# Kernel tuning notes

Hardware: AMD Instinct MI355X
Metric: run time of the kernel (lower is better)

The kernel has to match this reference:

```python
import jax, jax.numpy as jnp
import numpy as np

D_MODEL = 1024
NUM_HEADS = 16
MAX_LEN = 512  # chunk_size
BATCH = 2
SEQ_LEN = 2048


def _mha(x, w_in, b_in, w_out, b_out, num_heads):
    """torch.nn.MultiheadAttention (eval mode, self-attn) over the last-but-one axis.
    x: (..., S, d). Packed in-proj weight w_in: (3d, d), out-proj w_out: (d, d)."""
    *batch, S, d = x.shape
    hd = d // num_heads
    qkv = x @ w_in.T + b_in                      # (..., S, 3d)
    q, k, v = jnp.split(qkv, 3, axis=-1)
    def heads(t):
        return t.reshape(*batch, S, num_heads, hd)
    q, k, v = heads(q), heads(k), heads(v)
    scale = 1.0 / np.sqrt(hd).astype(np.float32)
    scores = jnp.einsum('...qhd,...khd->...hqk', q, k) * scale
    attn = jax.nn.softmax(scores, axis=-1)
    o = jnp.einsum('...hqk,...khd->...qhd', attn, v).reshape(*batch, S, d)
    return o @ w_out.T + b_out


def setup_inputs() -> dict:
    key = jax.random.key(0)
    ks = jax.random.split(key, 5)
    d = D_MODEL
    s = 0.02
    return {
        'x': jax.random.normal(ks[0], (BATCH, SEQ_LEN, d), dtype=jnp.float32),
        'w_in_l': jax.random.normal(ks[1], (3 * d, d), dtype=jnp.float32) * s,
        'b_in_l': jnp.zeros((3 * d,), jnp.float32),
        'w_out_l': jax.random.normal(ks[2], (d, d), dtype=jnp.float32) * s,
        'b_out_l': jnp.zeros((d,), jnp.float32),
        'w_in_g': jax.random.normal(ks[3], (3 * d, d), dtype=jnp.float32) * s,
        'b_in_g': jnp.zeros((3 * d,), jnp.float32),
        'w_out_g': jax.random.normal(ks[4], (d, d), dtype=jnp.float32) * s,
        'b_out_g': jnp.zeros((d,), jnp.float32),
    }


def reference(x, w_in_l, b_in_l, w_out_l, b_out_l, w_in_g, b_in_g, w_out_g, b_out_g):
    B, S, d = x.shape
    cs = MAX_LEN
    nc = S // cs
    # (B, nc, cs, d) -> (B, cs, nc, d): for each intra-chunk position, attend across chunks.
    xc = x.reshape(B, nc, cs, d).transpose(0, 2, 1, 3)
    # Vectorized replacement for the python loop over chunk positions:
    # batched MHA with batch (B, cs) and sequence length nc.
    loc = _mha(xc, w_in_l, b_in_l, w_out_l, b_out_l, NUM_HEADS)  # (B, cs, nc, d)
    # Faithful to torch: stack -> (nc, cs, B, d), transpose(1,2) -> (nc, B, cs, d),
    # then raw reshape to (B, S, d) (a layout-reinterpreting view, preserved here).
    loc = loc.transpose(2, 0, 1, 3).reshape(B, S, d)
    # Global full self-attention over the whole sequence.
    return _mha(loc, w_in_g, b_in_g, w_out_g, b_out_g, NUM_HEADS)
```

## Files before the change

### kernel.cpp

```cpp
#include <hip/hip_runtime.h>

#define BB 2
#define SS 2048
#define DD 1024
#define HH 16
#define HD 64
#define CS 512
#define NC 4
#define TD 3072
#define MM 4096

typedef __attribute__((ext_vector_type(8))) short short8;
typedef __attribute__((ext_vector_type(4))) float floatx4;

__device__ __forceinline__ float bf2f(unsigned short h) {
  union { unsigned int u; float f; } v; v.u = ((unsigned int)h) << 16; return v.f;
}
__device__ __forceinline__ unsigned short f2bf(float f) {
  union { float f; unsigned int u; } v; v.f = f;
  unsigned int r = (v.u + 0x7fffu + ((v.u >> 16) & 1u)) >> 16;
  return (unsigned short)r;
}
__device__ __forceinline__ short8 ld8f(const float* p) {
  floatx4 f0 = *(const floatx4*)p;
  floatx4 f1 = *(const floatx4*)(p + 4);
  short8 o;
  o[0] = (short)f2bf(f0[0]); o[1] = (short)f2bf(f0[1]);
  o[2] = (short)f2bf(f0[2]); o[3] = (short)f2bf(f0[3]);
  o[4] = (short)f2bf(f1[0]); o[5] = (short)f2bf(f1[1]);
  o[6] = (short)f2bf(f1[2]); o[7] = (short)f2bf(f1[3]);
  return o;
}
__device__ __forceinline__ short8 scale8_eighth(short8 a) {
  short8 o;
#pragma unroll
  for (int j = 0; j < 8; ++j) o[j] = (short)f2bf(bf2f((unsigned short)a[j]) * 0.125f);
  return o;
}
__device__ __forceinline__ void async16(const void* g, void* l) {
  __builtin_amdgcn_global_load_lds((const __attribute__((address_space(1))) void*)g,
                                   (__attribute__((address_space(3))) void*)l, 16, 0, 0);
}

__global__ __launch_bounds__(256) void cvt_bf16(const float* __restrict__ in,
                                                unsigned short* __restrict__ out, int n) {
  int i = (blockIdx.x * 256 + threadIdx.x) * 8;
  if (i < n) *(short8*)(out + i) = ld8f(in + i);
}

template <int W_F32, int C_F32>
__global__ __launch_bounds__(256) void gemm_bt_bias(
    const unsigned short* __restrict__ A, const void* __restrict__ Wv,
    const float* __restrict__ bias, void* __restrict__ Cv, int M, int N, int K) {
  __shared__ unsigned short sA[128 * 32];
  __shared__ unsigned short sB[128 * 32];
  const int tid = threadIdx.x;
  const int wid = tid >> 6, lane = tid & 63;
  const int quad = lane >> 4, l15 = lane & 15;
  const int wm = wid & 1, wn = wid >> 1;
  const int bm = blockIdx.y, bn = blockIdx.x;

  floatx4 acc[4][4];
#pragma unroll
  for (int i = 0; i < 4; ++i)
#pragma unroll
    for (int j = 0; j < 4; ++j) acc[i][j] = (floatx4){0.f, 0.f, 0.f, 0.f};

  const int r = tid >> 2;
  const int kc = (tid & 3) * 8;
  const unsigned short* gA = A + (size_t)(bm * 128 + r) * K + kc;
  const float*          gWf = (const float*)Wv          + (size_t)(bn * 128 + r) * K + kc;
  const unsigned short* gWh = (const unsigned short*)Wv + (size_t)(bn * 128 + r) * K + kc;
  unsigned short* lA = sA + wid * 512;
  unsigned short* lB = sB + wid * 512;

  for (int k0 = 0; k0 < K; k0 += 32) {
    async16(gA + k0, lA);
    async16(gA + (size_t)64 * K + k0, lA + 2048);
    if (W_F32) {
      short8 b0 = ld8f(gWf + k0);
      short8 b1 = ld8f(gWf + (size_t)64 * K + k0);
      *(short8*)(sB + r * 32 + kc) = b0;
      *(short8*)(sB + (64 + r) * 32 + kc) = b1;
    } else {
      async16(gWh + k0, lB);
      async16(gWh + (size_t)64 * K + k0, lB + 2048);
    }
    __syncthreads();

    short8 af[4], bfr[4];
#pragma unroll
    for (int i = 0; i < 4; ++i)
      af[i] = *(const short8*)(sA + (wm * 64 + i * 16 + l15) * 32 + quad * 8);
#pragma unroll
    for (int j = 0; j < 4; ++j)
      bfr[j] = *(const short8*)(sB + (wn * 64 + j * 16 + l15) * 32 + quad * 8);
#pragma unroll
    for (int i = 0; i < 4; ++i)
#pragma unroll
      for (int j = 0; j < 4; ++j)
        acc[i][j] = __builtin_amdgcn_mfma_f32_16x16x32_bf16(af[i], bfr[j], acc[i][j], 0, 0, 0);
    __syncthreads();
  }

#pragma unroll
  for (int j = 0; j < 4; ++j) {
    int n = bn * 128 + wn * 64 + j * 16 + l15;
    float bv = bias[n];
#pragma unroll
    for (int i = 0; i < 4; ++i) {
      int mrow = bm * 128 + wm * 64 + i * 16 + quad * 4;
#pragma unroll
      for (int rr = 0; rr < 4; ++rr) {
        float v = acc[i][j][rr] + bv;
        if (C_F32) ((float*)Cv)[(size_t)(mrow + rr) * N + n] = v;
        else ((unsigned short*)Cv)[(size_t)(mrow + rr) * N + n] = f2bf(v);
      }
    }
  }
}

__global__ __launch_bounds__(256) void attn_local(const unsigned short* __restrict__ QKV,
                                                  unsigned short* __restrict__ O) {
  const int tid = threadIdx.x;
  const int wid = tid >> 6, lane = tid & 63;
  const int idx = blockIdx.x * 4 + wid;
  const int h = idx & 15, c = (idx >> 4) & 511, b = idx >> 13;

  float q[NC], k[NC], v[NC];
#pragma unroll
  for (int n = 0; n < NC; ++n) {
    size_t base = (size_t)(b * SS + n * CS + c) * TD + h * HD + lane;
    q[n] = bf2f(QKV[base]);
    k[n] = bf2f(QKV[base + DD]);
    v[n] = bf2f(QKV[base + 2 * DD]);
  }
  float s[NC][NC];
#pragma unroll
  for (int m = 0; m < NC; ++m)
#pragma unroll
    for (int n = 0; n < NC; ++n) {
      float p = q[m] * k[n];
#pragma unroll
      for (int off = 32; off >= 1; off >>= 1) p += __shfl_xor(p, off);
      s[m][n] = p * 0.125f;
    }
#pragma unroll
  for (int m = 0; m < NC; ++m) {
    float mx = fmaxf(fmaxf(s[m][0], s[m][1]), fmaxf(s[m][2], s[m][3]));
    float e[NC], sum = 0.f;
#pragma unroll
    for (int n = 0; n < NC; ++n) { e[n] = __expf(s[m][n] - mx); sum += e[n]; }
    float o = (e[0] * v[0] + e[1] * v[1] + e[2] * v[2] + e[3] * v[3]) / sum;
    O[(size_t)(m * (BB * CS) + b * CS + c) * DD + h * HD + lane] = f2bf(o);
  }
}

__global__ __launch_bounds__(256) void transpose_v(const unsigned short* __restrict__ QKV,
                                                   unsigned short* __restrict__ VT) {
  __shared__ unsigned short sT[64 * 64];
  const int tid = threadIdx.x;
  const int bh = blockIdx.x, b = bh >> 4, h = bh & 15;
  const int s0 = blockIdx.y * 64;
#pragma unroll
  for (int it = 0; it < 2; ++it) {
    int C = it * 256 + tid;
    int t = C >> 3, dc = C & 7;
    short8 v = *(const short8*)(QKV + (size_t)(b * SS + s0 + t) * TD + 2 * DD + h * HD + dc * 8);
    *(short8*)(sT + t * 64 + ((dc ^ (t & 7)) << 3)) = v;
  }
  __syncthreads();
#pragma unroll
  for (int it = 0; it < 2; ++it) {
    int C = it * 256 + tid;
    int d = C >> 3, tc = C & 7;
    short8 o;
#pragma unroll
    for (int j = 0; j < 8; ++j) {
      int t = tc * 8 + j;
      o[j] = (short)sT[t * 64 + (((d >> 3) ^ (t & 7)) << 3) + (d & 7)];
    }
    *(short8*)(VT + ((size_t)(bh * 64 + d)) * SS + s0 + tc * 8) = o;
  }
}

__global__ __launch_bounds__(128) void attn_global(
    const unsigned short* __restrict__ Q, const unsigned short* __restrict__ Kp,
    const unsigned short* __restrict__ VT, unsigned short* __restrict__ O) {
  __shared__ unsigned short sK[64 * 64];
  __shared__ unsigned short sVT[64 * 64];
  __shared__ unsigned short sP[2][32 * 64];
  const int tid = threadIdx.x;
  const int wid = tid >> 6, lane = tid & 63;
  const int quad = lane >> 4, l15 = lane & 15;
  const int bh = blockIdx.x;
  const int b = bh >> 4, h = bh & 15;
  const int q0 = blockIdx.y * 64 + wid * 32;

  short8 qf[2][2];
#pragma unroll
  for (int g = 0; g < 2; ++g) {
    const unsigned short* qr = Q + (size_t)(b * SS + q0 + g * 16 + l15) * TD + h * HD + quad * 8;
    qf[g][0] = scale8_eighth(*(const short8*)qr);
    qf[g][1] = scale8_eighth(*(const short8*)(qr + 32));
  }

  float lsum[2][4];
  floatx4 oacc[2][4];
#pragma unroll
  for (int g = 0; g < 2; ++g)
#pragma unroll
    for (int s = 0; s < 4; ++s) { lsum[g][s] = 0.f; oacc[g][s] = (floatx4){0.f, 0.f, 0.f, 0.f}; }

  unsigned short* myP = &sP[wid][0];
  const unsigned short* vbase = VT + (size_t)(bh * 64) * SS;

  for (int kt = 0; kt < SS / 64; ++kt) {
    const int kbase = kt * 64;
#pragma unroll
    for (int it = 0; it < 4; ++it) {
      int P = it * 128 + tid;
      int key = P >> 3, dc = P & 7;
      short8 kv = *(const short8*)(Kp + (size_t)(b * SS + kbase + key) * TD + h * HD + dc * 8);
      *(short8*)(sK + key * 64 + ((dc ^ (key & 7)) << 3)) = kv;
    }
#pragma unroll
    for (int it = 0; it < 4; ++it) {
      int P = it * 128 + tid;
      int dim = P >> 3, kcc = P & 7;
      short8 vv = *(const short8*)(vbase + (size_t)dim * SS + kbase + kcc * 8);
      *(short8*)(sVT + dim * 64 + ((kcc ^ (dim & 7)) << 3)) = vv;
    }
    __syncthreads();

    floatx4 sacc[2][4];
#pragma unroll
    for (int sub = 0; sub < 4; ++sub) {
      int key = sub * 16 + l15;
      int c0 = (quad ^ (key & 7)) << 3;
      short8 kf0 = *(const short8*)(sK + key * 64 + c0);
      short8 kf1 = *(const short8*)(sK + key * 64 + (c0 ^ 32));
#pragma unroll
      for (int g = 0; g < 2; ++g) {
        floatx4 z = (floatx4){0.f, 0.f, 0.f, 0.f};
        z = __builtin_amdgcn_mfma_f32_16x16x32_bf16(qf[g][0], kf0, z, 0, 0, 0);
        z = __builtin_amdgcn_mfma_f32_16x16x32_bf16(qf[g][1], kf1, z, 0, 0, 0);
        sacc[g][sub] = z;
      }
    }

#pragma unroll
    for (int g = 0; g < 2; ++g)
#pragma unroll
      for (int sub = 0; sub < 4; ++sub) {
        int kc8 = sub * 2 + (l15 >> 3), k7 = l15 & 7;
#pragma unroll
        for (int rr = 0; rr < 4; ++rr) {
          unsigned int u = __float_as_uint(__expf(sacc[g][sub][rr]));
          lsum[g][rr] += __uint_as_float(u & 0xffff0000u);
          int row = g * 16 + quad * 4 + rr;
          myP[row * 64 + ((kc8 ^ (row & 7)) << 3) + k7] = (unsigned short)(u >> 16);
        }
      }
    __asm__ volatile("s_waitcnt lgkmcnt(0)" ::: "memory");

    short8 pf[2][2];
#pragma unroll
    for (int g = 0; g < 2; ++g) {
      int row = g * 16 + l15;
      int sw = row & 7;
#pragma unroll
      for (int c = 0; c < 2; ++c)
        pf[g][c] = *(const short8*)(myP + row * 64 + (((c * 4 + quad) ^ sw) << 3));
    }

#pragma unroll
    for (int sub = 0; sub < 4; ++sub) {
      int n = sub * 16 + l15;
      int v0 = (quad ^ (n & 7)) << 3;
      short8 vt0 = *(const short8*)(sVT + n * 64 + v0);
      short8 vt1 = *(const short8*)(sVT + n * 64 + (v0 ^ 32));
#pragma unroll
      for (int g = 0; g < 2; ++g) {
        oacc[g][sub] = __builtin_amdgcn_mfma_f32_16x16x32_bf16(pf[g][0], vt0, oacc[g][sub], 0, 0, 0);
        oacc[g][sub] = __builtin_amdgcn_mfma_f32_16x16x32_bf16(pf[g][1], vt1, oacc[g][sub], 0, 0, 0);
      }
    }
    __syncthreads();
  }

  float linv[2][4];
#pragma unroll
  for (int g = 0; g < 2; ++g)
#pragma unroll
    for (int rr = 0; rr < 4; ++rr) {
      float t = lsum[g][rr];
#pragma unroll
      for (int off = 8; off >= 1; off >>= 1) t += __shfl_xor(t, off);
      linv[g][rr] = 1.f / t;
    }
#pragma unroll
  for (int g = 0; g < 2; ++g)
#pragma unroll
    for (int sub = 0; sub < 4; ++sub)
#pragma unroll
      for (int rr = 0; rr < 4; ++rr) {
        int row = b * SS + q0 + g * 16 + quad * 4 + rr;
        O[(size_t)row * DD + h * HD + sub * 16 + l15] = f2bf(oacc[g][sub][rr] * linv[g][rr]);
      }
}

extern "C" void kernel_launch(void* const* d_in, const int* in_sizes, int n_in,
                              void* d_out, int out_size, void* d_ws, size_t ws_size,
                              hipStream_t stream) {
  const float* x       = (const float*)d_in[0];
  const float* w_in_l  = (const float*)d_in[1];
  const float* b_in_l  = (const float*)d_in[2];
  const float* w_out_l = (const float*)d_in[3];
  const float* b_out_l = (const float*)d_in[4];
  const float* w_in_g  = (const float*)d_in[5];
  const float* b_in_g  = (const float*)d_in[6];
  const float* w_out_g = (const float*)d_in[7];
  const float* b_out_g = (const float*)d_in[8];

  unsigned short* wsA = (unsigned short*)d_ws;
  unsigned short* wsB = wsA + (size_t)MM * TD;
  unsigned short* dob = (unsigned short*)d_out;
  unsigned short* wbf_out_l = dob;
  unsigned short* wbf_in_g  = dob + (size_t)DD * DD;
  unsigned short* wbf_in_l  = dob + 4 * (size_t)DD * DD;
  unsigned short* o1        = dob + 4 * (size_t)DD * DD;
  unsigned short* vtbuf     = dob;

  dim3 blk(256);
  cvt_bf16<<<dim3(DD * DD / 2048), blk, 0, stream>>>(w_out_l, wbf_out_l, DD * DD);
  cvt_bf16<<<dim3(TD * DD / 2048), blk, 0, stream>>>(w_in_g, wbf_in_g, TD * DD);
  cvt_bf16<<<dim3(TD * DD / 2048), blk, 0, stream>>>(w_in_l, wbf_in_l, TD * DD);
  cvt_bf16<<<dim3(MM * DD / 2048), blk, 0, stream>>>(x, wsB, MM * DD);

  gemm_bt_bias<0, 0><<<dim3(TD / 128, MM / 128), blk, 0, stream>>>(wsB, wbf_in_l, b_in_l, wsA, MM, TD, DD);
  attn_local<<<dim3(BB * CS * HH / 4), blk, 0, stream>>>(wsA, o1);
  gemm_bt_bias<0, 0><<<dim3(DD / 128, MM / 128), blk, 0, stream>>>(o1, wbf_out_l, b_out_l, wsB, MM, DD, DD);
  gemm_bt_bias<0, 0><<<dim3(TD / 128, MM / 128), blk, 0, stream>>>(wsB, wbf_in_g, b_in_g, wsA, MM, TD, DD);
  transpose_v<<<dim3(BB * HH, SS / 64), blk, 0, stream>>>(wsA, vtbuf);
  attn_global<<<dim3(BB * HH, SS / 64), dim3(128), 0, stream>>>(wsA, wsA + DD, vtbuf, wsB);
  cvt_bf16<<<dim3(DD * DD / 2048), blk, 0, stream>>>(w_out_g, wsA, DD * DD);
  gemm_bt_bias<0, 1><<<dim3(DD / 128, MM / 128), blk, 0, stream>>>(wsB, wsA, b_out_g, d_out, MM, DD, DD);
}
```

Before: 334.9 us.

## Split global attention keys across warps, shrink out-proj GEMM tiles, batch conversions

Global attention now runs 256-thread blocks in which two warp pairs each process half of the key range. The partial outputs and row sums are combined through shared memory at the end, which doubles the waves working per query tile. The output-projection GEMMs use 64-row M tiles so more blocks are launched for the N=1024 cases. The four weight/input fp32-to-bf16 conversions are merged into one launch. This costs extra LDS, an end-of-kernel reduction, and less A-tile reuse in the smaller GEMMs.

```diff
diff --git a/kernel.cpp b/kernel.cpp
--- a/kernel.cpp
+++ b/kernel.cpp
@@ -42,17 +42,33 @@
                                    (__attribute__((address_space(3))) void*)l, 16, 0, 0);
 }
 
+__global__ __launch_bounds__(256) void cvt_all(
+    const float* __restrict__ s0, unsigned short* __restrict__ d0, int n0,
+    const float* __restrict__ s1, unsigned short* __restrict__ d1, int n1,
+    const float* __restrict__ s2, unsigned short* __restrict__ d2, int n2,
+    const float* __restrict__ s3, unsigned short* __restrict__ d3, int n3) {
+  int bb = blockIdx.x;
+  const float* s; unsigned short* d; int off;
+  if (bb < n0) { s = s0; d = d0; off = bb; }
+  else if (bb < n0 + n1) { s = s1; d = d1; off = bb - n0; }
+  else if (bb < n0 + n1 + n2) { s = s2; d = d2; off = bb - n0 - n1; }
+  else { s = s3; d = d3; off = bb - n0 - n1 - n2; }
+  int i = (off * 256 + threadIdx.x) * 8;
+  *(short8*)(d + i) = ld8f(s + i);
+}
+
 __global__ __launch_bounds__(256) void cvt_bf16(const float* __restrict__ in,
                                                 unsigned short* __restrict__ out, int n) {
   int i = (blockIdx.x * 256 + threadIdx.x) * 8;
   if (i < n) *(short8*)(out + i) = ld8f(in + i);
 }
 
-template <int W_F32, int C_F32>
+template <int MT, int C_F32>
 __global__ __launch_bounds__(256) void gemm_bt_bias(
-    const unsigned short* __restrict__ A, const void* __restrict__ Wv,
+    const unsigned short* __restrict__ A, const unsigned short* __restrict__ W,
     const float* __restrict__ bias, void* __restrict__ Cv, int M, int N, int K) {
-  __shared__ unsigned short sA[128 * 32];
+  constexpr int AI = MT / 32;
+  __shared__ unsigned short sA[MT * 32];
   __shared__ unsigned short sB[128 * 32];
   const int tid = threadIdx.x;
   const int wid = tid >> 6, lane = tid & 63;
@@ -60,43 +76,36 @@
   const int wm = wid & 1, wn = wid >> 1;
   const int bm = blockIdx.y, bn = blockIdx.x;
 
-  floatx4 acc[4][4];
-#pragma unroll
-  for (int i = 0; i < 4; ++i)
+  floatx4 acc[AI][4];
+#pragma unroll
+  for (int i = 0; i < AI; ++i)
 #pragma unroll
     for (int j = 0; j < 4; ++j) acc[i][j] = (floatx4){0.f, 0.f, 0.f, 0.f};
 
   const int r = tid >> 2;
   const int kc = (tid & 3) * 8;
-  const unsigned short* gA = A + (size_t)(bm * 128 + r) * K + kc;
-  const float*          gWf = (const float*)Wv          + (size_t)(bn * 128 + r) * K + kc;
-  const unsigned short* gWh = (const unsigned short*)Wv + (size_t)(bn * 128 + r) * K + kc;
+  const unsigned short* gA = A + (size_t)(bm * MT + r) * K + kc;
+  const unsigned short* gW = W + (size_t)(bn * 128 + r) * K + kc;
   unsigned short* lA = sA + wid * 512;
   unsigned short* lB = sB + wid * 512;
 
   for (int k0 = 0; k0 < K; k0 += 32) {
-    async16(gA + k0, lA);
-    async16(gA + (size_t)64 * K + k0, lA + 2048);
-    if (W_F32) {
-      short8 b0 = ld8f(gWf + k0);
-      short8 b1 = ld8f(gWf + (size_t)64 * K + k0);
-      *(short8*)(sB + r * 32 + kc) = b0;
-      *(short8*)(sB + (64 + r) * 32 + kc) = b1;
-    } else {
-      async16(gWh + k0, lB);
-      async16(gWh + (size_t)64 * K + k0, lB + 2048);
-    }
+#pragma unroll
+    for (int s = 0; s < MT / 64; ++s)
+      async16(gA + (size_t)(s * 64) * K + k0, lA + s * 2048);
+    async16(gW + k0, lB);
+    async16(gW + (size_t)64 * K + k0, lB + 2048);
     __syncthreads();
 
-    short8 af[4], bfr[4];
-#pragma unroll
-    for (int i = 0; i < 4; ++i)
-      af[i] = *(const short8*)(sA + (wm * 64 + i * 16 + l15) * 32 + quad * 8);
+    short8 af[AI], bfr[4];
+#pragma unroll
+    for (int i = 0; i < AI; ++i)
+      af[i] = *(const short8*)(sA + (wm * (MT / 2) + i * 16 + l15) * 32 + quad * 8);
 #pragma unroll
     for (int j = 0; j < 4; ++j)
       bfr[j] = *(const short8*)(sB + (wn * 64 + j * 16 + l15) * 32 + quad * 8);
 #pragma unroll
-    for (int i = 0; i < 4; ++i)
+    for (int i = 0; i < AI; ++i)
 #pragma unroll
       for (int j = 0; j < 4; ++j)
         acc[i][j] = __builtin_amdgcn_mfma_f32_16x16x32_bf16(af[i], bfr[j], acc[i][j], 0, 0, 0);
@@ -108,8 +117,8 @@
     int n = bn * 128 + wn * 64 + j * 16 + l15;
     float bv = bias[n];
 #pragma unroll
-    for (int i = 0; i < 4; ++i) {
-      int mrow = bm * 128 + wm * 64 + i * 16 + quad * 4;
+    for (int i = 0; i < AI; ++i) {
+      int mrow = bm * MT + wm * (MT / 2) + i * 16 + quad * 4;
 #pragma unroll
       for (int rr = 0; rr < 4; ++rr) {
         float v = acc[i][j][rr] + bv;
@@ -184,18 +193,20 @@
   }
 }
 
-__global__ __launch_bounds__(128) void attn_global(
+__global__ __launch_bounds__(256) void attn_global(
     const unsigned short* __restrict__ Q, const unsigned short* __restrict__ Kp,
     const unsigned short* __restrict__ VT, unsigned short* __restrict__ O) {
-  __shared__ unsigned short sK[64 * 64];
-  __shared__ unsigned short sVT[64 * 64];
-  __shared__ unsigned short sP[2][32 * 64];
+  __shared__ unsigned short sK[2][64 * 64];
+  __shared__ unsigned short sVT[2][64 * 64];
+  __shared__ unsigned short sP[4][32 * 64];
+  __shared__ float lsumBuf[64];
   const int tid = threadIdx.x;
   const int wid = tid >> 6, lane = tid & 63;
   const int quad = lane >> 4, l15 = lane & 15;
+  const int qhalf = wid & 1, khalf = wid >> 1;
   const int bh = blockIdx.x;
   const int b = bh >> 4, h = bh & 15;
-  const int q0 = blockIdx.y * 64 + wid * 32;
+  const int q0 = blockIdx.y * 64 + qhalf * 32;
 
   short8 qf[2][2];
 #pragma unroll
@@ -213,23 +224,28 @@
     for (int s = 0; s < 4; ++s) { lsum[g][s] = 0.f; oacc[g][s] = (floatx4){0.f, 0.f, 0.f, 0.f}; }
 
   unsigned short* myP = &sP[wid][0];
+  const unsigned short* myK = &sK[khalf][0];
+  const unsigned short* myV = &sVT[khalf][0];
   const unsigned short* vbase = VT + (size_t)(bh * 64) * SS;
 
-  for (int kt = 0; kt < SS / 64; ++kt) {
-    const int kbase = kt * 64;
-#pragma unroll
-    for (int it = 0; it < 4; ++it) {
-      int P = it * 128 + tid;
-      int key = P >> 3, dc = P & 7;
-      short8 kv = *(const short8*)(Kp + (size_t)(b * SS + kbase + key) * TD + h * HD + dc * 8);
-      *(short8*)(sK + key * 64 + ((dc ^ (key & 7)) << 3)) = kv;
-    }
-#pragma unroll
-    for (int it = 0; it < 4; ++it) {
-      int P = it * 128 + tid;
-      int dim = P >> 3, kcc = P & 7;
-      short8 vv = *(const short8*)(vbase + (size_t)dim * SS + kbase + kcc * 8);
-      *(short8*)(sVT + dim * 64 + ((kcc ^ (dim & 7)) << 3)) = vv;
+  for (int t = 0; t < 16; ++t) {
+#pragma unroll
+    for (int kh = 0; kh < 2; ++kh) {
+      const int kbase = (kh * 16 + t) * 64;
+#pragma unroll
+      for (int it = 0; it < 2; ++it) {
+        int P = it * 256 + tid;
+        int key = P >> 3, dc = P & 7;
+        short8 kv = *(const short8*)(Kp + (size_t)(b * SS + kbase + key) * TD + h * HD + dc * 8);
+        *(short8*)(&sK[kh][0] + key * 64 + ((dc ^ (key & 7)) << 3)) = kv;
+      }
+#pragma unroll
+      for (int it = 0; it < 2; ++it) {
+        int P = it * 256 + tid;
+        int dim = P >> 3, kcc = P & 7;
+        short8 vv = *(const short8*)(vbase + (size_t)dim * SS + kbase + kcc * 8);
+        *(short8*)(&sVT[kh][0] + dim * 64 + ((kcc ^ (dim & 7)) << 3)) = vv;
+      }
     }
     __syncthreads();
 
@@ -238,8 +254,8 @@
     for (int sub = 0; sub < 4; ++sub) {
       int key = sub * 16 + l15;
       int c0 = (quad ^ (key & 7)) << 3;
-      short8 kf0 = *(const short8*)(sK + key * 64 + c0);
-      short8 kf1 = *(const short8*)(sK + key * 64 + (c0 ^ 32));
+      short8 kf0 = *(const short8*)(myK + key * 64 + c0);
+      short8 kf1 = *(const short8*)(myK + key * 64 + (c0 ^ 32));
 #pragma unroll
       for (int g = 0; g < 2; ++g) {
         floatx4 z = (floatx4){0.f, 0.f, 0.f, 0.f};
@@ -278,8 +294,8 @@
     for (int sub = 0; sub < 4; ++sub) {
       int n = sub * 16 + l15;
       int v0 = (quad ^ (n & 7)) << 3;
-      short8 vt0 = *(const short8*)(sVT + n * 64 + v0);
-      short8 vt1 = *(const short8*)(sVT + n * 64 + (v0 ^ 32));
+      short8 vt0 = *(const short8*)(myV + n * 64 + v0);
+      short8 vt1 = *(const short8*)(myV + n * 64 + (v0 ^ 32));
 #pragma unroll
       for (int g = 0; g < 2; ++g) {
         oacc[g][sub] = __builtin_amdgcn_mfma_f32_16x16x32_bf16(pf[g][0], vt0, oacc[g][sub], 0, 0, 0);
@@ -289,7 +305,7 @@
     __syncthreads();
   }
 
-  float linv[2][4];
+  float lred[2][4];
 #pragma unroll
   for (int g = 0; g < 2; ++g)
 #pragma unroll
@@ -297,17 +313,44 @@
       float t = lsum[g][rr];
 #pragma unroll
       for (int off = 8; off >= 1; off >>= 1) t += __shfl_xor(t, off);
-      linv[g][rr] = 1.f / t;
-    }
-#pragma unroll
-  for (int g = 0; g < 2; ++g)
-#pragma unroll
-    for (int sub = 0; sub < 4; ++sub)
-#pragma unroll
-      for (int rr = 0; rr < 4; ++rr) {
-        int row = b * SS + q0 + g * 16 + quad * 4 + rr;
-        O[(size_t)row * DD + h * HD + sub * 16 + l15] = f2bf(oacc[g][sub][rr] * linv[g][rr]);
-      }
+      lred[g][rr] = t;
+    }
+
+  float* obuf = (float*)&sP[0][0];
+  if (khalf == 1) {
+    float* my = obuf + qhalf * 2048;
+#pragma unroll
+    for (int g = 0; g < 2; ++g)
+#pragma unroll
+      for (int sub = 0; sub < 4; ++sub)
+#pragma unroll
+        for (int rr = 0; rr < 4; ++rr)
+          my[(g * 16 + quad * 4 + rr) * 64 + sub * 16 + l15] = oacc[g][sub][rr];
+    if (l15 == 0)
+#pragma unroll
+      for (int g = 0; g < 2; ++g)
+#pragma unroll
+        for (int rr = 0; rr < 4; ++rr)
+          lsumBuf[qhalf * 32 + g * 16 + quad * 4 + rr] = lred[g][rr];
+  }
+  __syncthreads();
+  if (khalf == 0) {
+    float* my = obuf + qhalf * 2048;
+#pragma unroll
+    for (int g = 0; g < 2; ++g) {
+#pragma unroll
+      for (int rr = 0; rr < 4; ++rr)
+        lred[g][rr] = 1.f / (lred[g][rr] + lsumBuf[qhalf * 32 + g * 16 + quad * 4 + rr]);
+#pragma unroll
+      for (int sub = 0; sub < 4; ++sub)
+#pragma unroll
+        for (int rr = 0; rr < 4; ++rr) {
+          float v = oacc[g][sub][rr] + my[(g * 16 + quad * 4 + rr) * 64 + sub * 16 + l15];
+          int row = b * SS + q0 + g * 16 + quad * 4 + rr;
+          O[(size_t)row * DD + h * HD + sub * 16 + l15] = f2bf(v * lred[g][rr]);
+        }
+    }
+  }
 }
 
 extern "C" void kernel_launch(void* const* d_in, const int* in_sizes, int n_in,
@@ -333,17 +376,17 @@
   unsigned short* vtbuf     = dob;
 
   dim3 blk(256);
-  cvt_bf16<<<dim3(DD * DD / 2048), blk, 0, stream>>>(w_out_l, wbf_out_l, DD * DD);
-  cvt_bf16<<<dim3(TD * DD / 2048), blk, 0, stream>>>(w_in_g, wbf_in_g, TD * DD);
-  cvt_bf16<<<dim3(TD * DD / 2048), blk, 0, stream>>>(w_in_l, wbf_in_l, TD * DD);
-  cvt_bf16<<<dim3(MM * DD / 2048), blk, 0, stream>>>(x, wsB, MM * DD);
-
-  gemm_bt_bias<0, 0><<<dim3(TD / 128, MM / 128), blk, 0, stream>>>(wsB, wbf_in_l, b_in_l, wsA, MM, TD, DD);
+  cvt_all<<<dim3(5632), blk, 0, stream>>>(w_out_l, wbf_out_l, 512,
+                                          w_in_g, wbf_in_g, 1536,
+                                          w_in_l, wbf_in_l, 1536,
+                                          x, wsB, 2048);
+
+  gemm_bt_bias<128, 0><<<dim3(TD / 128, MM / 128), blk, 0, stream>>>(wsB, wbf_in_l, b_in_l, wsA, MM, TD, DD);
   attn_local<<<dim3(BB * CS * HH / 4), blk, 0, stream>>>(wsA, o1);
-  gemm_bt_bias<0, 0><<<dim3(DD / 128, MM / 128), blk, 0, stream>>>(o1, wbf_out_l, b_out_l, wsB, MM, DD, DD);
-  gemm_bt_bias<0, 0><<<dim3(TD / 128, MM / 128), blk, 0, stream>>>(wsB, wbf_in_g, b_in_g, wsA, MM, TD, DD);
+  gemm_bt_bias<64, 0><<<dim3(DD / 128, MM / 64), blk, 0, stream>>>(o1, wbf_out_l, b_out_l, wsB, MM, DD, DD);
+  gemm_bt_bias<128, 0><<<dim3(TD / 128, MM / 128), blk, 0, stream>>>(wsB, wbf_in_g, b_in_g, wsA, MM, TD, DD);
   transpose_v<<<dim3(BB * HH, SS / 64), blk, 0, stream>>>(wsA, vtbuf);
-  attn_global<<<dim3(BB * HH, SS / 64), dim3(128), 0, stream>>>(wsA, wsA + DD, vtbuf, wsB);
+  attn_global<<<dim3(BB * HH, SS / 64), blk, 0, stream>>>(wsA, wsA + DD, vtbuf, wsB);
   cvt_bf16<<<dim3(DD * DD / 2048), blk, 0, stream>>>(w_out_g, wsA, DD * DD);
-  gemm_bt_bias<0, 1><<<dim3(DD / 128, MM / 128), blk, 0, stream>>>(wsB, wsA, b_out_g, d_out, MM, DD, DD);
-}
+  gemm_bt_bias<64, 1><<<dim3(DD / 128, MM / 64), blk, 0, stream>>>(wsB, wsA, b_out_g, d_out, MM, DD, DD);
+}
```

New measurement: 326.6 us. 1.03x faster.
